# Kernel tuning notes

Hardware: AMD Instinct MI355X
Metric: run time of the kernel (lower is better)

Reference implementation:

```python
import jax, jax.numpy as jnp
import numpy as np

SIGMA = 1.0

def setup_inputs() -> dict:
    key = jax.random.key(0)
    k1, k2, k3 = jax.random.split(key, 3)
    X_new = jax.random.normal(k1, (8192, 128), dtype=jnp.float32)
    X_train = jax.random.normal(k2, (32768, 128), dtype=jnp.float32)
    atomic_weights = jax.random.normal(k3, (32768, 1), dtype=jnp.float32)
    return {"X_new": X_new, "X_train": X_train, "atomic_weights": atomic_weights}

def reference(X_new, X_train, atomic_weights):
    x2 = jnp.sum(X_new * X_new, axis=-1, keepdims=True)            # [N_new, 1]
    y2 = jnp.sum(X_train * X_train, axis=-1)                       # [N_train]
    cross = jnp.einsum('nd,md->nm', X_new, X_train)                # [N_new, N_train]
    dist_sq = jnp.maximum(x2 + y2[None, :] - 2.0 * cross, 0.0)
    K_new = jnp.exp(-dist_sq / (2.0 * SIGMA ** 2))
    per_atom_energy = K_new @ atomic_weights                       # [N_new, 1]
    return per_atom_energy
```

## Files before the change

kernel.cpp:

```cpp
#include <hip/hip_runtime.h>
#include <stdint.h>

typedef __attribute__((ext_vector_type(4))) int i32x4;
typedef __attribute__((ext_vector_type(16))) int i32x16;
typedef __attribute__((ext_vector_type(8))) short short8;
typedef __attribute__((ext_vector_type(16))) float f32x16;

#define LOG2E 1.4426950408889634f
#define S1 16.0f
#define S1_INV 0.0625f
#define S2 4096.0f
#define K2 (1.0f / 65536.0f)

__device__ inline float fast_exp2(float x) {
#if __has_builtin(__builtin_amdgcn_exp2f)
  return __builtin_amdgcn_exp2f(x);
#else
  float r;
  asm("v_exp_f32 %0, %1" : "=v"(r) : "v"(x));
  return r;
#endif
}

__device__ inline void gload16(const void* g, void* l) {
  __builtin_amdgcn_global_load_lds(
      (const __attribute__((address_space(1))) void*)g,
      (__attribute__((address_space(3))) void*)l, 16, 0, 0);
}
__device__ inline void gload4(const void* g, void* l) {
  __builtin_amdgcn_global_load_lds(
      (const __attribute__((address_space(1))) void*)g,
      (__attribute__((address_space(3))) void*)l, 4, 0, 0);
}

__device__ inline void q4(float4 v, float pre, int& hw, int& lw) {
  float xs[4] = {v.x, v.y, v.z, v.w};
  int h = 0, l = 0;
#pragma unroll
  for (int j = 0; j < 4; ++j) {
    float x = xs[j] * pre;
    float hf = rintf(fminf(fmaxf(x * S1, -127.f), 127.f));
    float rf = x - hf * S1_INV;
    float lf = rintf(fminf(fmaxf(rf * S2, -127.f), 127.f));
    h |= ((int)hf & 255) << (8 * j);
    l |= ((int)lf & 255) << (8 * j);
  }
  hw = h;
  lw = l;
}

__global__ __launch_bounds__(256) void gk_conv_s(const float* __restrict__ Xtr,
                                                 const float* __restrict__ wts,
                                                 char* __restrict__ planes,
                                                 float* __restrict__ s, int M) {
  int g = blockIdx.x * 256 + threadIdx.x;
  int row = g >> 3;
  int gr = g & 7;
  if (row >= M) return;
  const float* p = Xtr + (size_t)row * 128 + gr * 16;
  int hw[4], lw[4];
  float ss = 0.f;
#pragma unroll
  for (int i = 0; i < 4; ++i) {
    float4 v = *(const float4*)(p + i * 4);
    ss += v.x * v.x + v.y * v.y + v.z * v.z + v.w * v.w;
    q4(v, 1.0f, hw[i], lw[i]);
  }
  ss += __shfl_xor(ss, 1, 64);
  ss += __shfl_xor(ss, 2, 64);
  ss += __shfl_xor(ss, 4, 64);
  if (gr == 0) s[row] = expf(-0.5f * ss) * wts[row];

  int T = row >> 5, r = row & 31;
  size_t base = (size_t)T * 8192 + (gr >> 1) * 1024 + (gr & 1) * 512 + r * 16;
  *(i32x4*)(planes + base) = (i32x4){hw[0], hw[1], hw[2], hw[3]};
  *(i32x4*)(planes + base + 4096) = (i32x4){lw[0], lw[1], lw[2], lw[3]};
}

__global__ __launch_bounds__(256, 4) void gk_main_i8(
    const float* __restrict__ Xnew, const char* __restrict__ planes,
    const float* __restrict__ s, float* __restrict__ out, int N, int M,
    int mchunk) {
  extern __shared__ char dlds[];

  const int t = threadIdx.x;
  const int l = t & 63;
  const int w = t >> 6;
  const int cl = l & 31;
  const int lk = l >> 5;

  const int n0 = blockIdx.x * 128;
  const int M0 = blockIdx.y * mchunk;
  const int iters = mchunk >> 5;
  const int T0 = M0 >> 5;

#define STAGE(tt)                                                       \
  {                                                                     \
    int st_ = ((tt) < iters) ? (tt) : (iters - 1);   \
    const char* src_ = planes + (size_t)(T0 + st_) * 8192 + t * 16;     \
    char* dst_ = dlds + ((tt)&3) * 8192 + t * 16;                       \
    gload16(src_, dst_);                                                \
    gload16(src_ + 4096, dst_ + 4096);                                  \
    gload4(s + M0 + st_ * 32 + l, dlds + 32768 + ((tt)&3) * 256);       \
  }

#define MFMAS_Z(acc_hh, acc_m, tile)                                    \
  {                                                                     \
    const char* buf_ = dlds + ((tile)&3) * 8192;                        \
    {                                                                   \
      const char* kb_ = buf_ + lk * 512 + cl * 16;                      \
      i32x4 ah_ = *(const i32x4*)(kb_);                                 \
      i32x4 al_ = *(const i32x4*)(kb_ + 4096);                          \
      acc_hh = __builtin_amdgcn_mfma_i32_32x32x32_i8(ah_, bh[0], zc, 0, 0, 0);      \
      acc_m = __builtin_amdgcn_mfma_i32_32x32x32_i8(ah_, bl[0], zc, 0, 0, 0);       \
      acc_m = __builtin_amdgcn_mfma_i32_32x32x32_i8(al_, bh[0], acc_m, 0, 0, 0);    \
    }                                                                   \
    _Pragma("unroll") for (int kf = 1; kf < 4; ++kf) {                  \
      const char* kb_ = buf_ + kf * 1024 + lk * 512 + cl * 16;          \
      i32x4 ah_ = *(const i32x4*)(kb_);                                 \
      i32x4 al_ = *(const i32x4*)(kb_ + 4096);                          \
      acc_hh = __builtin_amdgcn_mfma_i32_32x32x32_i8(ah_, bh[kf], acc_hh, 0, 0, 0); \
      acc_m = __builtin_amdgcn_mfma_i32_32x32x32_i8(ah_, bl[kf], acc_m, 0, 0, 0);   \
      acc_m = __builtin_amdgcn_mfma_i32_32x32x32_i8(al_, bh[kf], acc_m, 0, 0, 0);   \
    }                                                                   \
  }

#define EPI(acc_hh, acc_m, tile)                                        \
  {                                                                     \
    const float4* sl4_ =                                                \
        (const float4*)(dlds + 32768 + ((tile)&3) * 256);               \
    _Pragma("unroll") for (int q = 0; q < 4; ++q) {                     \
      float4 sv_ = sl4_[q * 2 + lk];                                    \
      _Pragma("unroll") for (int j = 0; j < 4; ++j) {                   \
        int r_ = q * 4 + j;                                             \
        float c_ = (float)((acc_hh[r_] << 8) + acc_m[r_]) * K2;         \
        out0 += fast_exp2(c_) * (&sv_.x)[j];                            \
      }                                                                 \
    }                                                                   \
  }

#define REGION_END                                                      \
  asm volatile("s_waitcnt vmcnt(3)" ::: "memory");                      \
  __builtin_amdgcn_s_barrier();

  STAGE(0);
  STAGE(1);

  i32x4 bh[4], bl[4];
  float pref;
  {
    float ss = 0.f;
    const float* pc = Xnew + (size_t)(n0 + w * 32 + cl) * 128;
#pragma unroll
    for (int kf = 0; kf < 4; ++kf) {
      const float* p = pc + kf * 32 + lk * 16;
      int hw[4], lw[4];
#pragma unroll
      for (int i = 0; i < 4; ++i) {
        float4 v = *(const float4*)(p + i * 4);
        ss += v.x * v.x + v.y * v.y + v.z * v.z + v.w * v.w;
        q4(v, LOG2E, hw[i], lw[i]);
      }
      bh[kf] = (i32x4){hw[0], hw[1], hw[2], hw[3]};
      bl[kf] = (i32x4){lw[0], lw[1], lw[2], lw[3]};
    }
    ss += __shfl_xor(ss, 32, 64);
    pref = expf(-0.5f * ss);
  }

  float out0 = 0.f;
  const i32x16 zc = {0, 0, 0, 0, 0, 0, 0, 0, 0, 0, 0, 0, 0, 0, 0, 0};
  i32x16 hh, m;

  asm volatile("s_waitcnt vmcnt(3)" ::: "memory");
  __builtin_amdgcn_s_barrier();

#pragma unroll 1
  for (int it = 0; it < iters; ++it) {
    __builtin_amdgcn_sched_barrier(0);
    STAGE(it + 2);
    MFMAS_Z(hh, m, it);
    EPI(hh, m, it);
    REGION_END;
  }

  out0 += __shfl_xor(out0, 32, 64);
  if (l < 32) {
    int n = n0 + w * 32 + l;
    atomicAdd(out + n, pref * out0);
  }
#undef STAGE
#undef MFMAS_Z
#undef EPI
#undef REGION_END
}

__global__ __launch_bounds__(256) void gk_prep(
    const float* __restrict__ Xnew, const float* __restrict__ Xtr,
    const float* __restrict__ w, float* __restrict__ s,
    float* __restrict__ pref, int M, int N) {
  int row = blockIdx.x * 4 + (threadIdx.x >> 6);
  int lane = threadIdx.x & 63;
  if (row >= M + N) return;
  const float* src =
      (row < M) ? (Xtr + (size_t)row * 128) : (Xnew + (size_t)(row - M) * 128);
  float2 v = *(const float2*)(src + lane * 2);
  float ss = v.x * v.x + v.y * v.y;
#pragma unroll
  for (int o = 32; o >= 1; o >>= 1) ss += __shfl_xor(ss, o, 64);
  if (lane == 0) {
    float e = expf(-0.5f * ss);
    if (row < M)
      s[row] = e * w[row];
    else
      pref[row - M] = e;
  }
}

__device__ inline unsigned swz_fb(unsigned off) {
  return off ^ (((off >> 8) & 7u) << 4);
}
__device__ inline void split8(float x0, float x1, float x2, float x3,
                              float x4, float x5, float x6, float x7,
                              float scale, short8& hi, short8& lo) {
  float xs[8] = {x0, x1, x2, x3, x4, x5, x6, x7};
#pragma unroll
  for (int i = 0; i < 8; ++i) {
    float v = xs[i] * scale;
    unsigned u = __float_as_uint(v);
    float hf = __uint_as_float(u & 0xffff0000u);
    float rr = v - hf;
    hi[i] = (short)(u >> 16);
    lo[i] = (short)(__float_as_uint(rr) >> 16);
  }
}

__global__ __launch_bounds__(256, 2) void gk_main_fb(
    const float* __restrict__ Xnew, const float* __restrict__ Xtr,
    const float* __restrict__ s, const float* __restrict__ pref,
    float* __restrict__ out, int N, int M, int mchunk) {
  __shared__ __attribute__((aligned(16))) char lds[33024];
  const int t = threadIdx.x;
  const int l = t & 63;
  const int w = t >> 6;
  const int lrow = l & 31;
  const int lk = l >> 5;
  const int n0 = blockIdx.x * 256;
  const int M0 = blockIdx.y * mchunk;
  const int iters = mchunk >> 6;

  short8 bh[2][8], bl[2][8];
  {
    const int colbase = n0 + w * 64;
#pragma unroll
    for (int nf = 0; nf < 2; ++nf) {
      int col = colbase + nf * 32 + lrow;
      const float* p = Xnew + (size_t)col * 128 + lk * 8;
#pragma unroll
      for (int kf = 0; kf < 8; ++kf) {
        float4 f0 = *(const float4*)(p + kf * 16);
        float4 f1 = *(const float4*)(p + kf * 16 + 4);
        split8(f0.x, f0.y, f0.z, f0.w, f1.x, f1.y, f1.z, f1.w, LOG2E,
               bh[nf][kf], bl[nf][kf]);
      }
    }
  }

  float out0 = 0.f, out1 = 0.f;
  float4 ga[4][2];
  float sreg = 0.f;
  {
    const float* abase = Xtr + (size_t)M0 * 128;
#pragma unroll
    for (int j = 0; j < 4; ++j) {
      int c = t + j * 256;
      int row = c >> 4, oct = c & 15;
      const float* p = abase + (size_t)row * 128 + oct * 8;
      ga[j][0] = *(const float4*)p;
      ga[j][1] = *(const float4*)(p + 4);
    }
    if (t < 64) sreg = s[M0 + t];
  }

#pragma unroll 1
  for (int it = 0; it < iters; ++it) {
    __syncthreads();
#pragma unroll
    for (int j = 0; j < 4; ++j) {
      int c = t + j * 256;
      int row = c >> 4, oct = c & 15;
      unsigned off = swz_fb((unsigned)(row * 256 + oct * 16));
      short8 hi, lo;
      split8(ga[j][0].x, ga[j][0].y, ga[j][0].z, ga[j][0].w, ga[j][1].x,
             ga[j][1].y, ga[j][1].z, ga[j][1].w, 1.0f, hi, lo);
      *(short8*)(lds + off) = hi;
      *(short8*)(lds + 16384 + off) = lo;
    }
    if (t < 64) *(float*)(lds + 32768 + t * 4) = sreg;
    __syncthreads();
    if (it + 1 < iters) {
      const float* abase = Xtr + (size_t)(M0 + (it + 1) * 64) * 128;
#pragma unroll
      for (int j = 0; j < 4; ++j) {
        int c = t + j * 256;
        int row = c >> 4, oct = c & 15;
        const float* p = abase + (size_t)row * 128 + oct * 8;
        ga[j][0] = *(const float4*)p;
        ga[j][1] = *(const float4*)(p + 4);
      }
      if (t < 64) sreg = s[M0 + (it + 1) * 64 + t];
    }
#pragma unroll
    for (int mf = 0; mf < 2; ++mf) {
      f32x16 acc0 = {0, 0, 0, 0, 0, 0, 0, 0, 0, 0, 0, 0, 0, 0, 0, 0};
      f32x16 acc1 = {0, 0, 0, 0, 0, 0, 0, 0, 0, 0, 0, 0, 0, 0, 0, 0};
#pragma unroll
      for (int kf = 0; kf < 8; ++kf) {
        unsigned off =
            swz_fb((unsigned)((mf * 32 + lrow) * 256 + kf * 32 + lk * 16));
        short8 ah = *(const short8*)(lds + off);
        short8 al = *(const short8*)(lds + 16384 + off);
        acc0 = __builtin_amdgcn_mfma_f32_32x32x16_bf16(ah, bh[0][kf], acc0, 0, 0, 0);
        acc1 = __builtin_amdgcn_mfma_f32_32x32x16_bf16(ah, bh[1][kf], acc1, 0, 0, 0);
        acc0 = __builtin_amdgcn_mfma_f32_32x32x16_bf16(ah, bl[0][kf], acc0, 0, 0, 0);
        acc1 = __builtin_amdgcn_mfma_f32_32x32x16_bf16(ah, bl[1][kf], acc1, 0, 0, 0);
        acc0 = __builtin_amdgcn_mfma_f32_32x32x16_bf16(al, bh[0][kf], acc0, 0, 0, 0);
        acc1 = __builtin_amdgcn_mfma_f32_32x32x16_bf16(al, bh[1][kf], acc1, 0, 0, 0);
      }
      const float* sl = (const float*)(lds + 32768 + mf * 128);
#pragma unroll
      for (int r = 0; r < 16; ++r) {
        int row = (r & 3) + 8 * (r >> 2) + 4 * lk;
        float sv = sl[row];
        out0 += fast_exp2(acc0[r]) * sv;
        out1 += fast_exp2(acc1[r]) * sv;
      }
    }
  }
  out0 += __shfl_xor(out0, 32, 64);
  out1 += __shfl_xor(out1, 32, 64);
  if (l < 32) {
    int n = n0 + w * 64 + l;
    atomicAdd(out + n, pref[n] * out0);
    n += 32;
    atomicAdd(out + n, pref[n] * out1);
  }
}

extern "C" void kernel_launch(void* const* d_in, const int* in_sizes, int n_in,
                              void* d_out, int out_size, void* d_ws,
                              size_t ws_size, hipStream_t stream) {
  const float* Xnew = (const float*)d_in[0];
  const float* Xtr = (const float*)d_in[1];
  const float* wts = (const float*)d_in[2];
  float* out = (float*)d_out;

  const int N = in_sizes[0] / 128;
  const int M = in_sizes[1] / 128;

  char* ws = (char*)d_ws;
  float* s_ws = (float*)ws;
  char* planes_ws = ws + (size_t)M * 4;
  const size_t need = (size_t)M * 4 + (size_t)M * 256;

  hipMemsetAsync(d_out, 0, (size_t)N * sizeof(float), stream);

  if (ws_size >= need) {
    gk_conv_s<<<dim3(M * 8 / 256), 256, 0, stream>>>(Xtr, wts, planes_ws,
                                                     s_ws, M);
    const int SPLIT = 16;
    dim3 grid(N / 128, SPLIT);
    gk_main_i8<<<grid, 256, 33792, stream>>>(Xnew, planes_ws, s_ws, out, N, M,
                                             M / SPLIT);
  } else {
    float* pref_ws = s_ws + M;
    int rows = M + N;
    gk_prep<<<dim3((rows + 3) / 4), 256, 0, stream>>>(Xnew, Xtr, wts, s_ws,
                                                      pref_ws, M, N);
    const int SPLIT = 16;
    dim3 grid(N / 256, SPLIT);
    gk_main_fb<<<grid, 256, 0, stream>>>(Xnew, Xtr, s_ws, pref_ws, out, N, M,
                                         M / SPLIT);
  }
}
```

Measured before the change: 131.4 us.

## Process two 32-row train tiles per iteration with triple-buffered LDS staging

The main int8 MFMA loop now handles 64 training rows per iteration: two independent accumulator sets, with the LDS ring changed from 4x8KB to 3x16KB. The intent is to halve the barriers and wait points per row and give the MFMA and exp epilogue more independent work to overlap. The M split drops from 16 to 12, using a rounded chunk size with a clamped end. Launch bounds drop to 3 blocks per CU to fit the larger LDS and register footprint, so occupancy is lower.

```diff
diff --git a/kernel.cpp b/kernel.cpp
--- a/kernel.cpp
+++ b/kernel.cpp
@@ -77,7 +77,7 @@
   *(i32x4*)(planes + base + 4096) = (i32x4){lw[0], lw[1], lw[2], lw[3]};
 }
 
-__global__ __launch_bounds__(256, 4) void gk_main_i8(
+__global__ __launch_bounds__(256, 3) void gk_main_i8(
     const float* __restrict__ Xnew, const char* __restrict__ planes,
     const float* __restrict__ s, float* __restrict__ out, int N, int M,
     int mchunk) {
@@ -91,57 +91,71 @@
 
   const int n0 = blockIdx.x * 128;
   const int M0 = blockIdx.y * mchunk;
-  const int iters = mchunk >> 5;
-  const int T0 = M0 >> 5;
-
-#define STAGE(tt)                                                       \
+  const int Mend = (M0 + mchunk < M) ? (M0 + mchunk) : M;
+  const int P = (Mend - M0) >> 6;
+  const int T0p = M0 >> 6;
+
+#define ZERO16 ((i32x16){0, 0, 0, 0, 0, 0, 0, 0, 0, 0, 0, 0, 0, 0, 0, 0})
+
+#define STAGE(pp)                                                       \
   {                                                                     \
-    int st_ = ((tt) < iters) ? (tt) : (iters - 1);   \
-    const char* src_ = planes + (size_t)(T0 + st_) * 8192 + t * 16;     \
-    char* dst_ = dlds + ((tt)&3) * 8192 + t * 16;                       \
+    int st_ = ((pp) < P) ? (pp) : (P - 1);           \
+    const char* src_ = planes + (size_t)(T0p + st_) * 16384 + t * 16;   \
+    char* dst_ = dlds + ((pp) % 3) * 16384 + t * 16;                    \
     gload16(src_, dst_);                                                \
     gload16(src_ + 4096, dst_ + 4096);                                  \
-    gload4(s + M0 + st_ * 32 + l, dlds + 32768 + ((tt)&3) * 256);       \
-  }
-
-#define MFMAS_Z(acc_hh, acc_m, tile)                                    \
+    gload16(src_ + 8192, dst_ + 8192);                                  \
+    gload16(src_ + 12288, dst_ + 12288);                                \
+    gload4(s + M0 + st_ * 64 + l, dlds + 49152 + ((pp) % 3) * 256);     \
+  }
+
+#define MFMAS_Z(hA, mA, hB, mB, pp)                                     \
   {                                                                     \
-    const char* buf_ = dlds + ((tile)&3) * 8192;                        \
+    const char* buf_ = dlds + ((pp) % 3) * 16384;                       \
     {                                                                   \
-      const char* kb_ = buf_ + lk * 512 + cl * 16;                      \
-      i32x4 ah_ = *(const i32x4*)(kb_);                                 \
-      i32x4 al_ = *(const i32x4*)(kb_ + 4096);                          \
-      acc_hh = __builtin_amdgcn_mfma_i32_32x32x32_i8(ah_, bh[0], zc, 0, 0, 0);      \
-      acc_m = __builtin_amdgcn_mfma_i32_32x32x32_i8(ah_, bl[0], zc, 0, 0, 0);       \
-      acc_m = __builtin_amdgcn_mfma_i32_32x32x32_i8(al_, bh[0], acc_m, 0, 0, 0);    \
+      const char* k0_ = buf_ + lk * 512 + cl * 16;                      \
+      i32x4 a0h_ = *(const i32x4*)(k0_);                                \
+      i32x4 a0l_ = *(const i32x4*)(k0_ + 4096);                         \
+      i32x4 a1h_ = *(const i32x4*)(k0_ + 8192);                         \
+      i32x4 a1l_ = *(const i32x4*)(k0_ + 12288);                        \
+      hA = __builtin_amdgcn_mfma_i32_32x32x32_i8(a0h_, bh[0], zc, 0, 0, 0);      \
+      mA = __builtin_amdgcn_mfma_i32_32x32x32_i8(a0h_, bl[0], zc, 0, 0, 0);      \
+      mA = __builtin_amdgcn_mfma_i32_32x32x32_i8(a0l_, bh[0], mA, 0, 0, 0);      \
+      hB = __builtin_amdgcn_mfma_i32_32x32x32_i8(a1h_, bh[0], zc, 0, 0, 0);      \
+      mB = __builtin_amdgcn_mfma_i32_32x32x32_i8(a1h_, bl[0], zc, 0, 0, 0);      \
+      mB = __builtin_amdgcn_mfma_i32_32x32x32_i8(a1l_, bh[0], mB, 0, 0, 0);      \
     }                                                                   \
     _Pragma("unroll") for (int kf = 1; kf < 4; ++kf) {                  \
-      const char* kb_ = buf_ + kf * 1024 + lk * 512 + cl * 16;          \
-      i32x4 ah_ = *(const i32x4*)(kb_);                                 \
-      i32x4 al_ = *(const i32x4*)(kb_ + 4096);                          \
-      acc_hh = __builtin_amdgcn_mfma_i32_32x32x32_i8(ah_, bh[kf], acc_hh, 0, 0, 0); \
-      acc_m = __builtin_amdgcn_mfma_i32_32x32x32_i8(ah_, bl[kf], acc_m, 0, 0, 0);   \
-      acc_m = __builtin_amdgcn_mfma_i32_32x32x32_i8(al_, bh[kf], acc_m, 0, 0, 0);   \
+      const char* k0_ = buf_ + kf * 1024 + lk * 512 + cl * 16;          \
+      i32x4 a0h_ = *(const i32x4*)(k0_);                                \
+      i32x4 a0l_ = *(const i32x4*)(k0_ + 4096);                         \
+      i32x4 a1h_ = *(const i32x4*)(k0_ + 8192);                         \
+      i32x4 a1l_ = *(const i32x4*)(k0_ + 12288);                        \
+      hA = __builtin_amdgcn_mfma_i32_32x32x32_i8(a0h_, bh[kf], hA, 0, 0, 0);     \
+      mA = __builtin_amdgcn_mfma_i32_32x32x32_i8(a0h_, bl[kf], mA, 0, 0, 0);     \
+      mA = __builtin_amdgcn_mfma_i32_32x32x32_i8(a0l_, bh[kf], mA, 0, 0, 0);     \
+      hB = __builtin_amdgcn_mfma_i32_32x32x32_i8(a1h_, bh[kf], hB, 0, 0, 0);     \
+      mB = __builtin_amdgcn_mfma_i32_32x32x32_i8(a1h_, bl[kf], mB, 0, 0, 0);     \
+      mB = __builtin_amdgcn_mfma_i32_32x32x32_i8(a1l_, bh[kf], mB, 0, 0, 0);     \
     }                                                                   \
   }
 
-#define EPI(acc_hh, acc_m, tile)                                        \
+#define EPI2(hA, mA, hB, mB, pp)                                        \
   {                                                                     \
     const float4* sl4_ =                                                \
-        (const float4*)(dlds + 32768 + ((tile)&3) * 256);               \
+        (const float4*)(dlds + 49152 + ((pp) % 3) * 256);               \
     _Pragma("unroll") for (int q = 0; q < 4; ++q) {                     \
-      float4 sv_ = sl4_[q * 2 + lk];                                    \
+      float4 sv0_ = sl4_[q * 2 + lk];                                   \
+      float4 sv1_ = sl4_[8 + q * 2 + lk];                               \
       _Pragma("unroll") for (int j = 0; j < 4; ++j) {                   \
         int r_ = q * 4 + j;                                             \
-        float c_ = (float)((acc_hh[r_] << 8) + acc_m[r_]) * K2;         \
-        out0 += fast_exp2(c_) * (&sv_.x)[j];                            \
+        float cA_ = (float)((hA[r_] << 8) + mA[r_]) * K2;               \
+        float cB_ = (float)((hB[r_] << 8) + mB[r_]) * K2;               \
+        out0 += fast_exp2(cA_) * (&sv0_.x)[j];                          \
+        out0 += fast_exp2(cB_) * (&sv1_.x)[j];                          \
       }                                                                 \
     }                                                                   \
   }
-
-#define REGION_END                                                      \
-  asm volatile("s_waitcnt vmcnt(3)" ::: "memory");                      \
-  __builtin_amdgcn_s_barrier();
 
   STAGE(0);
   STAGE(1);
@@ -169,19 +183,20 @@
   }
 
   float out0 = 0.f;
-  const i32x16 zc = {0, 0, 0, 0, 0, 0, 0, 0, 0, 0, 0, 0, 0, 0, 0, 0};
-  i32x16 hh, m;
-
-  asm volatile("s_waitcnt vmcnt(3)" ::: "memory");
+  const i32x16 zc = ZERO16;
+  i32x16 hA, mA, hB, mB;
+
+  asm volatile("s_waitcnt vmcnt(5)" ::: "memory");
   __builtin_amdgcn_s_barrier();
 
 #pragma unroll 1
-  for (int it = 0; it < iters; ++it) {
+  for (int p = 0; p < P; ++p) {
     __builtin_amdgcn_sched_barrier(0);
-    STAGE(it + 2);
-    MFMAS_Z(hh, m, it);
-    EPI(hh, m, it);
-    REGION_END;
+    STAGE(p + 2);
+    MFMAS_Z(hA, mA, hB, mB, p);
+    EPI2(hA, mA, hB, mB, p);
+    asm volatile("s_waitcnt vmcnt(5)" ::: "memory");
+    __builtin_amdgcn_s_barrier();
   }
 
   out0 += __shfl_xor(out0, 32, 64);
@@ -191,8 +206,8 @@
   }
 #undef STAGE
 #undef MFMAS_Z
-#undef EPI
-#undef REGION_END
+#undef EPI2
+#undef ZERO16
 }
 
 __global__ __launch_bounds__(256) void gk_prep(
@@ -368,10 +383,11 @@
   if (ws_size >= need) {
     gk_conv_s<<<dim3(M * 8 / 256), 256, 0, stream>>>(Xtr, wts, planes_ws,
                                                      s_ws, M);
-    const int SPLIT = 16;
+    const int SPLIT = 12;
+    const int CH = ((M + SPLIT - 1) / SPLIT + 63) & ~63;
     dim3 grid(N / 128, SPLIT);
-    gk_main_i8<<<grid, 256, 33792, stream>>>(Xnew, planes_ws, s_ws, out, N, M,
-                                             M / SPLIT);
+    gk_main_i8<<<grid, 256, 49920, stream>>>(Xnew, planes_ws, s_ws, out, N, M,
+                                             CH);
   } else {
     float* pref_ws = s_ws + M;
     int rows = M + N;
```

Measured after the change: 131.1 us. No clear change (-0.2%).
